# Performance work log

Hardware: AMD Instinct MI355X
Metric: run time of the kernel (lower is better)

The kernel has to match this reference:

```python
import jax, jax.numpy as jnp
import numpy as np

EPS = 1e-5
K = 2  # superpatch hop


def _bn(x, gamma, beta, mean, var):
    # inference-mode BatchNorm2d over channel dim (NCHW)
    inv = gamma / jnp.sqrt(var + EPS)
    return x * inv[None, :, None, None] + (beta - mean * inv)[None, :, None, None]


def _conv1x1(x, w, b):
    # x: [B,C,H,W], w: [O,C], b: [O]
    return jnp.einsum('bchw,oc->bohw', x, w) + b[None, :, None, None]


def setup_inputs() -> dict:
    key = jax.random.key(0)
    ks = jax.random.split(key, 24)
    B, C, H, W = 32, 192, 56, 56
    r = lambda k, shape, s=0.05: jax.random.normal(k, shape, dtype=jnp.float32) * s
    pv = lambda k, shape: jax.random.uniform(k, shape, dtype=jnp.float32, minval=0.5, maxval=1.5)
    inp = {
        'x': jax.random.normal(ks[0], (B, C, H, W), dtype=jnp.float32),
        # RepCPE: depthwise 7x7 conv, groups=C -> weight [C,1,7,7]
        'cpe_w': r(ks[1], (C, 1, 7, 7)),
        'cpe_b': r(ks[2], (C,)),
        # fc1: 1x1 conv C->C + BN
        'fc1_w': r(ks[3], (C, C)), 'fc1_b': r(ks[4], (C,)),
        'bn1_g': pv(ks[5], (C,)), 'bn1_b': r(ks[6], (C,)),
        'bn1_m': r(ks[7], (C,), 0.1), 'bn1_v': pv(ks[8], (C,)),
        # graph_conv.nn: 1x1 conv 2C->C + BN + GELU
        'gc_w': r(ks[9], (C, 2 * C)), 'gc_b': r(ks[10], (C,)),
        'bng_g': pv(ks[11], (C,)), 'bng_b': r(ks[12], (C,)),
        'bng_m': r(ks[13], (C,), 0.1), 'bng_v': pv(ks[14], (C,)),
        # fc2: 1x1 conv C->C + BN
        'fc2_w': r(ks[15], (C, C)), 'fc2_b': r(ks[16], (C,)),
        'bn2_g': pv(ks[17], (C,)), 'bn2_b': r(ks[18], (C,)),
        'bn2_m': r(ks[19], (C,), 0.1), 'bn2_v': pv(ks[20], (C,)),
    }
    return inp


def reference(x, cpe_w, cpe_b, fc1_w, fc1_b, bn1_g, bn1_b, bn1_m, bn1_v,
              gc_w, gc_b, bng_g, bng_b, bng_m, bng_v,
              fc2_w, fc2_b, bn2_g, bn2_b, bn2_m, bn2_v):
    C = x.shape[1]
    # --- RepCPE: depthwise 7x7 conv + bias, residual add ---
    pe = jax.lax.conv_general_dilated(
        x, cpe_w, window_strides=(1, 1), padding='SAME',
        feature_group_count=C,
        dimension_numbers=('NCHW', 'OIHW', 'NCHW'))
    x = pe + cpe_b[None, :, None, None] + x
    # --- fc1: 1x1 conv + BN ---
    x = _bn(_conv1x1(x, fc1_w, fc1_b), bn1_g, bn1_b, bn1_m, bn1_v)
    # --- MRConv4d: max-relative over 4 shifted neighbor views ---
    # torch.cat([x[..., -K:, :], x[..., :-K, :]], dim=2) == roll(+K) along H, etc.
    d = jnp.maximum(jnp.roll(x, K, axis=2) - x, jnp.roll(x, -K, axis=2) - x)
    d = jnp.maximum(d, jnp.roll(x, K, axis=3) - x)
    x_j = jnp.maximum(jnp.maximum(d, jnp.roll(x, -K, axis=3) - x), 0.0)  # x_j init = x - x = 0
    xc = jnp.concatenate([x, x_j], axis=1)  # [B,2C,H,W]
    x = jax.nn.gelu(_bn(_conv1x1(xc, gc_w, gc_b), bng_g, bng_b, bng_m, bng_v),
                    approximate=False)
    # --- fc2: 1x1 conv + BN ---
    x = _bn(_conv1x1(x, fc2_w, fc2_b), bn2_g, bn2_b, bn2_m, bn2_v)
    return x
```

## Files before the change

kernel.cpp:

```cpp
#include <hip/hip_runtime.h>
#include <hip/hip_bf16.h>


#define CC   192
#define HW   3136
#define NB   32

using short8 = __attribute__((ext_vector_type(8))) short;
using f32x4  = __attribute__((ext_vector_type(4))) float;

__device__ __forceinline__ float bf2f(short s) {
  union { unsigned u; float f; } x; x.u = ((unsigned)(unsigned short)s) << 16; return x.f;
}
__device__ __forceinline__ short f2bf(float f) {
  __hip_bfloat16 h = __float2bfloat16(f);
  return *reinterpret_cast<short*>(&h);
}
__device__ __forceinline__ float geluf(float v) {
  float u = 0.7978845608028654f * (v + 0.044715f * v * v * v);
  float e = __expf(2.0f * u);
  return 0.5f * v * (2.0f - 2.0f / (e + 1.0f));
}
__device__ __forceinline__ void gl2lds(const char* g, char* l) {
  __builtin_amdgcn_global_load_lds(
      (const __attribute__((address_space(1))) void*)g,
      (__attribute__((address_space(3))) void*)l, 16, 0, 0);
}

__global__ void __launch_bounds__(256) fold_kernel(
    const float* __restrict__ fc1_w, const float* __restrict__ fc1_b,
    const float* __restrict__ bn1_g, const float* __restrict__ bn1_b,
    const float* __restrict__ bn1_m, const float* __restrict__ bn1_v,
    const float* __restrict__ gc_w,  const float* __restrict__ gc_b,
    const float* __restrict__ bng_g, const float* __restrict__ bng_b,
    const float* __restrict__ bng_m, const float* __restrict__ bng_v,
    const float* __restrict__ fc2_w, const float* __restrict__ fc2_b,
    const float* __restrict__ bn2_g, const float* __restrict__ bn2_b,
    const float* __restrict__ bn2_m, const float* __restrict__ bn2_v,
    __hip_bfloat16* __restrict__ W1f, __hip_bfloat16* __restrict__ Wgf, __hip_bfloat16* __restrict__ W2f,
    float* __restrict__ b1f, float* __restrict__ bgf, float* __restrict__ b2f) {
  int gt = blockIdx.x * 256 + threadIdx.x;
  if (gt < 3 * CC) {
    int which = gt / CC, o = gt - which * CC;
    const float *G, *Bt, *M, *V, *Bi; float* dst;
    if (which == 0)      { G = bn1_g; Bt = bn1_b; M = bn1_m; V = bn1_v; Bi = fc1_b; dst = b1f; }
    else if (which == 1) { G = bng_g; Bt = bng_b; M = bng_m; V = bng_v; Bi = gc_b;  dst = bgf; }
    else                 { G = bn2_g; Bt = bn2_b; M = bn2_m; V = bn2_v; Bi = fc2_b; dst = b2f; }
    float inv = G[o] * rsqrtf(V[o] + 1e-5f);
    dst[o] = Bi[o] * inv + Bt[o] - M[o] * inv;
  }
  int i = gt;
  if (i < CC * CC) {
    int o = i / CC;
    float inv = bn1_g[o] * rsqrtf(bn1_v[o] + 1e-5f);
    W1f[i] = __float2bfloat16(fc1_w[i] * inv);
  } else if (i < CC * CC + CC * 2 * CC) {
    int j = i - CC * CC; int o = j / (2 * CC);
    float inv = bng_g[o] * rsqrtf(bng_v[o] + 1e-5f);
    Wgf[j] = __float2bfloat16(gc_w[j] * inv);
  } else if (i < CC * CC * 4) {
    int j = i - CC * CC * 3; int o = j / CC;
    float inv = bn2_g[o] * rsqrtf(bn2_v[o] + 1e-5f);
    W2f[j] = __float2bfloat16(fc2_w[j] * inv);
  }
}

#define CSTR 956
__global__ void __launch_bounds__(256, 4) dwconv_kernel(
    const float* __restrict__ x, const float* __restrict__ cw,
    const float* __restrict__ cb, __hip_bfloat16* __restrict__ y0pm) {
  __shared__ short in_t[16 * CSTR];
  const int t = threadIdx.x;
  int bb = blockIdx.x;
  const int rs = bb % 7;  bb /= 7;
  const int cg = bb % 12; bb /= 12;
  const int b  = bb;
  const int h0 = rs * 8;

  for (int i = t; i < 16 * CSTR / 8; i += 256) ((int4*)in_t)[i] = int4{0, 0, 0, 0};
  __syncthreads();

  for (int it = t; it < 16 * 14 * 14; it += 256) {
    int w4 = it % 14, rr = (it / 14) % 14, c = it / 196;
    int gh = h0 - 3 + rr;
    if (gh >= 0 && gh < 56) {
      float4 v = *(const float4*)(x + ((size_t)(b * CC + cg * 16 + c) * 56 + gh) * 56 + w4 * 4);
      short4 s4 = { f2bf(v.x), f2bf(v.y), f2bf(v.z), f2bf(v.w) };
      *(short4*)(in_t + c * CSTR + rr * 68 + 4 + w4 * 4) = s4;
    }
  }
  __syncthreads();

  const int c = t & 15, g = t >> 4;
  const int cgx = g % 7, rh = g / 7;
  if (g < 14) {
    const float* wp = cw + (cg * 16 + c) * 49;
    const float bias = cb[cg * 16 + c];
    const short* base = in_t + c * CSTR + rh * 4 * 68 + cgx * 8;
    float acc[4][8] = {};
    float wr[7], wn[7];
#pragma unroll
    for (int i = 0; i < 7; ++i) wr[i] = wp[i];
#pragma unroll
    for (int kh = 0; kh < 7; ++kh) {
      if (kh < 6) {
#pragma unroll
        for (int i = 0; i < 7; ++i) wn[i] = wp[(kh + 1) * 7 + i];
      }
      if (kh == 3) wr[3] += 1.0f;
#pragma unroll
      for (int r = 0; r < 4; ++r) {
        const short* rp = base + (r + kh) * 68;
        int2 q0 = *(const int2*)(rp);
        int2 q1 = *(const int2*)(rp + 4);
        int2 q2 = *(const int2*)(rp + 8);
        int2 q3 = *(const int2*)(rp + 12);
        int dw[8] = { q0.x, q0.y, q1.x, q1.y, q2.x, q2.y, q3.x, q3.y };
        float v[16];
#pragma unroll
        for (int q = 0; q < 8; ++q) {
          union { int i; float f; } lo, hi;
          lo.i = dw[q] << 16; hi.i = dw[q] & 0xffff0000;
          v[q * 2] = lo.f; v[q * 2 + 1] = hi.f;
        }
#pragma unroll
        for (int kw = 0; kw < 7; ++kw) {
          float wv = wr[kw];
#pragma unroll
          for (int ww = 0; ww < 8; ++ww)
            acc[r][ww] = fmaf(wv, v[ww + kw + 1], acc[r][ww]);
        }
      }
#pragma unroll
      for (int i = 0; i < 7; ++i) wr[i] = wn[i];
    }
    short* dst = (short*)y0pm + ((size_t)b * HW + (size_t)(h0 + rh * 4) * 56 + cgx * 8) * CC
                 + cg * 16 + c;
#pragma unroll
    for (int r = 0; r < 4; ++r)
#pragma unroll
      for (int ww = 0; ww < 8; ++ww)
        dst[(size_t)(r * 56 + ww) * CC] = f2bf(acc[r][ww] + bias);
  }
}

__device__ __forceinline__ void xj_load(short8 (&nb)[5], const short* y1c, int hwl) {
  int h = hwl / 56, w = hwl - h * 56;
  int hp = (h >= 54) ? h - 54 : h + 2;
  int hm = (h < 2) ? h + 54 : h - 2;
  int wp = (w >= 54) ? w - 54 : w + 2;
  int wm = (w < 2) ? w + 54 : w - 2;
  nb[0] = *(const short8*)(y1c + (size_t)hwl * CC);
  nb[1] = *(const short8*)(y1c + (size_t)(hp * 56 + w) * CC);
  nb[2] = *(const short8*)(y1c + (size_t)(hm * 56 + w) * CC);
  nb[3] = *(const short8*)(y1c + (size_t)(h * 56 + wp) * CC);
  nb[4] = *(const short8*)(y1c + (size_t)(h * 56 + wm) * CC);
}
__device__ __forceinline__ void xj_write(char* dst, const short8 (&nb)[5], int dstoff) {
  short8 res;
#pragma unroll
  for (int q = 0; q < 8; ++q) {
    float m = fmaxf(fmaxf(bf2f(nb[1][q]), bf2f(nb[2][q])),
                    fmaxf(bf2f(nb[3][q]), bf2f(nb[4][q])));
    res[q] = f2bf(fmaxf(m - bf2f(nb[0][q]), 0.0f));
  }
  *(short8*)(dst + dstoff) = res;
}

template<int MODE>
__global__ void __launch_bounds__(256, 2) gemm_kernel(
    const __hip_bfloat16* __restrict__ actA,
    const __hip_bfloat16* __restrict__ Wf, const float* __restrict__ bfv,
    void* __restrict__ outp) {
  __shared__ char smem[2][24576];
  const int t = threadIdx.x;
  const int lane = t & 63, w = t >> 6;
  const int lrow = lane & 15, lhi = lane >> 4;
  constexpr int NT = NB * 49;

  int goff[6];
#pragma unroll
  for (int j = 0; j < 6; ++j) {
    int idx = j * 4096 + t * 16;
    int p = idx / 384, qd = idx - p * 384;
    goff[j] = p * 384 + (qd ^ ((p & 7) << 4));
  }

  float bw0[3];
  float bw2[3][4];
  if (MODE != 2) {
#pragma unroll
    for (int wi = 0; wi < 3; ++wi) bw0[wi] = bfv[w * 48 + wi * 16 + lrow];
  } else {
#pragma unroll
    for (int wi = 0; wi < 3; ++wi)
#pragma unroll
      for (int r = 0; r < 4; ++r) bw2[wi][r] = bfv[w * 48 + wi * 16 + lhi * 4 + r];
  }

  short8 wreg[6][3];
#pragma unroll
  for (int kk = 0; kk < 6; ++kk)
#pragma unroll
    for (int wi = 0; wi < 3; ++wi) {
      int o = w * 48 + wi * 16 + lrow;
      wreg[kk][wi] = *(const short8*)((const short*)Wf + (size_t)o * 192 + kk * 32 + lhi * 8);
    }

  const int step = gridDim.x;
  int tile = blockIdx.x;
  {
    const char* src = (const char*)actA + (size_t)tile * 24576;
#pragma unroll
    for (int j = 0; j < 6; ++j)
      gl2lds(src + goff[j], smem[0] + j * 4096 + w * 1024);
  }
  __syncthreads();
  int cur = 0;

  while (tile < NT) {
    const int tnext = tile + step;
    f32x4 acc[4][3] = {};
    if (tnext < NT) {
      const char* nsrc = (const char*)actA + (size_t)tnext * 24576;
#pragma unroll
      for (int j = 0; j < 6; ++j)
        gl2lds(nsrc + goff[j], smem[cur ^ 1] + j * 4096 + w * 1024);
    }
#pragma unroll
    for (int kk = 0; kk < 6; ++kk) {
      short8 af[4];
#pragma unroll
      for (int ai = 0; ai < 4; ++ai) {
        int p = ai * 16 + lrow;
        af[ai] = *(const short8*)(smem[cur] + p * 384 + ((kk * 64 + lhi * 16) ^ ((p & 7) << 4)));
      }
#pragma unroll
      for (int ai = 0; ai < 4; ++ai)
#pragma unroll
        for (int wi = 0; wi < 3; ++wi)
          acc[ai][wi] = (MODE == 2)
              ? __builtin_amdgcn_mfma_f32_16x16x32_bf16(wreg[kk][wi], af[ai], acc[ai][wi], 0, 0, 0)
              : __builtin_amdgcn_mfma_f32_16x16x32_bf16(af[ai], wreg[kk][wi], acc[ai][wi], 0, 0, 0);
    }
    __syncthreads();
    cur ^= 1;

    if (MODE != 2) {
      short* ob = (short*)outp + (size_t)tile * 64 * CC;
#pragma unroll
      for (int wi = 0; wi < 3; ++wi) {
        int o = w * 48 + wi * 16 + lrow;
#pragma unroll
        for (int ai = 0; ai < 4; ++ai)
#pragma unroll
          for (int r = 0; r < 4; ++r) {
            int p = ai * 16 + lhi * 4 + r;
            ob[(size_t)p * CC + o] = f2bf(acc[ai][wi][r] + bw0[wi]);
          }
      }
    } else {
      int bimg = tile / 49, hwbase = (tile - bimg * 49) * 64;
      float* ob = (float*)outp + (size_t)bimg * CC * HW + hwbase;
#pragma unroll
      for (int wi = 0; wi < 3; ++wi)
#pragma unroll
        for (int r = 0; r < 4; ++r) {
          int o = w * 48 + wi * 16 + lhi * 4 + r;
#pragma unroll
          for (int ai = 0; ai < 4; ++ai)
            ob[(size_t)o * HW + ai * 16 + lrow] = acc[ai][wi][r] + bw2[wi][r];
        }
    }
    tile = tnext;
  }
}

__global__ void __launch_bounds__(768, 3) gemm2_kernel(
    const __hip_bfloat16* __restrict__ y1g, const __hip_bfloat16* __restrict__ Wf,
    const float* __restrict__ bfv, __hip_bfloat16* __restrict__ outp) {
  __shared__ char smem[2][24576];
  const int t = threadIdx.x;
  const int lane = t & 63, w = t >> 6;
  const int lrow = lane & 15, lhi = lane >> 4;
  constexpr int NT = NB * 49;

  int sp[2], sq[2], goff[2];
#pragma unroll
  for (int j = 0; j < 2; ++j) {
    int idx = j * 12288 + t * 16;
    sp[j] = idx / 384;
    sq[j] = idx - sp[j] * 384;
    goff[j] = sp[j] * 384 + (sq[j] ^ ((sp[j] & 7) << 4));
  }

  const float bw = bfv[w * 16 + lrow];

  short8 wreg[2][6];
#pragma unroll
  for (int c = 0; c < 2; ++c)
#pragma unroll
    for (int kk = 0; kk < 6; ++kk) {
      int o = w * 16 + lrow;
      wreg[c][kk] = *(const short8*)((const short*)Wf +
          (size_t)o * 384 + c * 192 + kk * 32 + lhi * 8);
    }

  const int step = gridDim.x;
  int tile = blockIdx.x;
  {
    const char* src = (const char*)y1g + (size_t)tile * 24576;
#pragma unroll
    for (int j = 0; j < 2; ++j)
      gl2lds(src + goff[j], smem[0] + j * 12288 + w * 1024);
  }
  __syncthreads();
  int cur = 0;

  while (tile < NT) {
    const int tnext = tile + step;
    const int bimg = tile / 49;
    const int hwbase = (tile - bimg * 49) * 64;
    const short* y1b = (const short*)y1g + (size_t)bimg * HW * CC;
    f32x4 acc[4] = {};

#pragma unroll
    for (int j = 0; j < 2; ++j) {
      short8 nb[5];
      xj_load(nb, y1b + (sq[j] >> 1), hwbase + sp[j]);
      xj_write(smem[cur ^ 1], nb, goff[j]);
    }
#pragma unroll
    for (int kk = 0; kk < 6; ++kk) {
      short8 af[4];
#pragma unroll
      for (int ai = 0; ai < 4; ++ai) {
        int p = ai * 16 + lrow;
        af[ai] = *(const short8*)(smem[cur] + p * 384 + ((kk * 64 + lhi * 16) ^ ((p & 7) << 4)));
      }
#pragma unroll
      for (int ai = 0; ai < 4; ++ai)
        acc[ai] = __builtin_amdgcn_mfma_f32_16x16x32_bf16(af[ai], wreg[0][kk], acc[ai], 0, 0, 0);
    }
    __syncthreads();
    cur ^= 1;

    if (tnext < NT) {
      const char* nsrc = (const char*)y1g + (size_t)tnext * 24576;
#pragma unroll
      for (int j = 0; j < 2; ++j)
        gl2lds(nsrc + goff[j], smem[cur ^ 1] + j * 12288 + w * 1024);
    }
#pragma unroll
    for (int kk = 0; kk < 6; ++kk) {
      short8 af[4];
#pragma unroll
      for (int ai = 0; ai < 4; ++ai) {
        int p = ai * 16 + lrow;
        af[ai] = *(const short8*)(smem[cur] + p * 384 + ((kk * 64 + lhi * 16) ^ ((p & 7) << 4)));
      }
#pragma unroll
      for (int ai = 0; ai < 4; ++ai)
        acc[ai] = __builtin_amdgcn_mfma_f32_16x16x32_bf16(af[ai], wreg[1][kk], acc[ai], 0, 0, 0);
    }
    __syncthreads();
    cur ^= 1;

    short* ob = (short*)outp + (size_t)tile * 64 * CC;
    const int o = w * 16 + lrow;
#pragma unroll
    for (int ai = 0; ai < 4; ++ai)
#pragma unroll
      for (int r = 0; r < 4; ++r) {
        int p = ai * 16 + lhi * 4 + r;
        ob[(size_t)p * CC + o] = f2bf(geluf(acc[ai][r] + bw));
      }
    tile = tnext;
  }
}

extern "C" void kernel_launch(void* const* d_in, const int* in_sizes, int n_in,
                              void* d_out, int out_size, void* d_ws, size_t ws_size,
                              hipStream_t stream) {
  const float* x     = (const float*)d_in[0];
  const float* cpe_w = (const float*)d_in[1];
  const float* cpe_b = (const float*)d_in[2];
  const float* fc1_w = (const float*)d_in[3];
  const float* fc1_b = (const float*)d_in[4];
  const float* bn1_g = (const float*)d_in[5];
  const float* bn1_b = (const float*)d_in[6];
  const float* bn1_m = (const float*)d_in[7];
  const float* bn1_v = (const float*)d_in[8];
  const float* gc_w  = (const float*)d_in[9];
  const float* gc_b  = (const float*)d_in[10];
  const float* bng_g = (const float*)d_in[11];
  const float* bng_b = (const float*)d_in[12];
  const float* bng_m = (const float*)d_in[13];
  const float* bng_v = (const float*)d_in[14];
  const float* fc2_w = (const float*)d_in[15];
  const float* fc2_b = (const float*)d_in[16];
  const float* bn2_g = (const float*)d_in[17];
  const float* bn2_b = (const float*)d_in[18];
  const float* bn2_m = (const float*)d_in[19];
  const float* bn2_v = (const float*)d_in[20];

  if (ws_size < 77594624) return;
  char* ws = (char*)d_ws;
  __hip_bfloat16* W1f = (__hip_bfloat16*)(ws);
  __hip_bfloat16* Wgf = (__hip_bfloat16*)(ws + 73728);
  __hip_bfloat16* W2f = (__hip_bfloat16*)(ws + 221184);
  float* b1f = (float*)(ws + 294912);
  float* bgf = (float*)(ws + 295680);
  float* b2f = (float*)(ws + 296448);
  __hip_bfloat16* y0  = (__hip_bfloat16*)(ws + 524288);
  __hip_bfloat16* y1  = (__hip_bfloat16*)d_out;
  float* out = (float*)d_out;

  fold_kernel<<<576, 256, 0, stream>>>(fc1_w, fc1_b, bn1_g, bn1_b, bn1_m, bn1_v,
      gc_w, gc_b, bng_g, bng_b, bng_m, bng_v, fc2_w, fc2_b, bn2_g, bn2_b, bn2_m, bn2_v,
      W1f, Wgf, W2f, b1f, bgf, b2f);
  dwconv_kernel<<<NB * 12 * 7, 256, 0, stream>>>(x, cpe_w, cpe_b, y0);
  gemm_kernel<0><<<512, 256, 0, stream>>>(y0, W1f, b1f, y1);
  gemm2_kernel<<<512, 768, 0, stream>>>(y1, Wgf, bgf, y0);
  gemm_kernel<2><<<512, 256, 0, stream>>>(y0, W2f, b2f, out);
}
```

Baseline: 146.4 us.

## Pack channel pairs in LDS and use packed FP32 FMA in depthwise conv

The depthwise 7x7 conv kernel now stores two channels interleaved as bf16 pairs per 32-bit LDS word and computes both channels at once with v_pk_fma_f32 through inline asm. Each thread handles a channel pair over 2 rows by 8 columns instead of one channel over 4 rows, and 224 of the 256 threads do work instead of 224 before. The aim is to halve the FMA instruction count, widen LDS reads, and write output as packed 32-bit stores. The cost is more LDS reads per output, since each thread covers fewer rows and the 6 halo rows are reloaded more often relative to the outputs produced.

```diff
diff --git a/kernel.cpp b/kernel.cpp
--- a/kernel.cpp
+++ b/kernel.cpp
@@ -8,6 +8,7 @@
 
 using short8 = __attribute__((ext_vector_type(8))) short;
 using f32x4  = __attribute__((ext_vector_type(4))) float;
+using f32x2  = __attribute__((ext_vector_type(2))) float;
 
 __device__ __forceinline__ float bf2f(short s) {
   union { unsigned u; float f; } x; x.u = ((unsigned)(unsigned short)s) << 16; return x.f;
@@ -15,6 +16,19 @@
 __device__ __forceinline__ short f2bf(float f) {
   __hip_bfloat16 h = __float2bfloat16(f);
   return *reinterpret_cast<short*>(&h);
+}
+__device__ __forceinline__ unsigned pack_bf2(float a, float b) {
+  return ((unsigned)(unsigned short)f2bf(a)) | (((unsigned)(unsigned short)f2bf(b)) << 16);
+}
+__device__ __forceinline__ f32x2 up2(unsigned d) {
+  union { unsigned u; float f; } lo, hi;
+  lo.u = d << 16; hi.u = d & 0xffff0000u;
+  f32x2 r; r.x = lo.f; r.y = hi.f; return r;
+}
+__device__ __forceinline__ f32x2 pk_fma(f32x2 a, f32x2 b, f32x2 c) {
+  f32x2 d;
+  asm("v_pk_fma_f32 %0, %1, %2, %3" : "=v"(d) : "v"(a), "v"(b), "v"(c));
+  return d;
 }
 __device__ __forceinline__ float geluf(float v) {
   float u = 0.7978845608028654f * (v + 0.044715f * v * v * v);
@@ -65,11 +79,10 @@
   }
 }
 
-#define CSTR 956
 __global__ void __launch_bounds__(256, 4) dwconv_kernel(
     const float* __restrict__ x, const float* __restrict__ cw,
     const float* __restrict__ cb, __hip_bfloat16* __restrict__ y0pm) {
-  __shared__ short in_t[16 * CSTR];
+  __shared__ unsigned in_t2[8 * 956];
   const int t = threadIdx.x;
   int bb = blockIdx.x;
   const int rs = bb % 7;  bb /= 7;
@@ -77,70 +90,77 @@
   const int b  = bb;
   const int h0 = rs * 8;
 
-  for (int i = t; i < 16 * CSTR / 8; i += 256) ((int4*)in_t)[i] = int4{0, 0, 0, 0};
+  for (int i = t; i < 1912; i += 256) ((uint4*)in_t2)[i] = uint4{0, 0, 0, 0};
   __syncthreads();
 
-  for (int it = t; it < 16 * 14 * 14; it += 256) {
-    int w4 = it % 14, rr = (it / 14) % 14, c = it / 196;
+  for (int it = t; it < 8 * 14 * 14; it += 256) {
+    int w4 = it % 14, rr = (it / 14) % 14, cp = it / 196;
     int gh = h0 - 3 + rr;
     if (gh >= 0 && gh < 56) {
-      float4 v = *(const float4*)(x + ((size_t)(b * CC + cg * 16 + c) * 56 + gh) * 56 + w4 * 4);
-      short4 s4 = { f2bf(v.x), f2bf(v.y), f2bf(v.z), f2bf(v.w) };
-      *(short4*)(in_t + c * CSTR + rr * 68 + 4 + w4 * 4) = s4;
+      const float* pa = x + ((size_t)(b * CC + cg * 16 + cp * 2) * 56 + gh) * 56 + w4 * 4;
+      float4 va = *(const float4*)pa;
+      float4 vb = *(const float4*)(pa + 3136);
+      uint4 u;
+      u.x = pack_bf2(va.x, vb.x); u.y = pack_bf2(va.y, vb.y);
+      u.z = pack_bf2(va.z, vb.z); u.w = pack_bf2(va.w, vb.w);
+      *(uint4*)(in_t2 + cp * 956 + rr * 68 + 4 + w4 * 4) = u;
     }
   }
   __syncthreads();
 
-  const int c = t & 15, g = t >> 4;
-  const int cgx = g % 7, rh = g / 7;
-  if (g < 14) {
-    const float* wp = cw + (cg * 16 + c) * 49;
-    const float bias = cb[cg * 16 + c];
-    const short* base = in_t + c * CSTR + rh * 4 * 68 + cgx * 8;
-    float acc[4][8] = {};
-    float wr[7], wn[7];
-#pragma unroll
-    for (int i = 0; i < 7; ++i) wr[i] = wp[i];
+  const int cp = t & 7, g = t >> 3;
+  const int cgx = g % 7, rq = g / 7;
+  if (g < 28) {
+    const float* wpA = cw + (cg * 16 + cp * 2) * 49;
+    f32x2 bias2;
+    bias2.x = cb[cg * 16 + cp * 2];
+    bias2.y = cb[cg * 16 + cp * 2 + 1];
+    const unsigned* base = in_t2 + cp * 956 + rq * 2 * 68 + cgx * 8;
+    f32x2 acc2[2][8] = {};
+    f32x2 wr2[7], wn2[7];
+#pragma unroll
+    for (int i = 0; i < 7; ++i) { wr2[i].x = wpA[i]; wr2[i].y = wpA[49 + i]; }
 #pragma unroll
     for (int kh = 0; kh < 7; ++kh) {
       if (kh < 6) {
 #pragma unroll
-        for (int i = 0; i < 7; ++i) wn[i] = wp[(kh + 1) * 7 + i];
-      }
-      if (kh == 3) wr[3] += 1.0f;
-#pragma unroll
-      for (int r = 0; r < 4; ++r) {
-        const short* rp = base + (r + kh) * 68;
-        int2 q0 = *(const int2*)(rp);
-        int2 q1 = *(const int2*)(rp + 4);
-        int2 q2 = *(const int2*)(rp + 8);
-        int2 q3 = *(const int2*)(rp + 12);
-        int dw[8] = { q0.x, q0.y, q1.x, q1.y, q2.x, q2.y, q3.x, q3.y };
-        float v[16];
-#pragma unroll
-        for (int q = 0; q < 8; ++q) {
-          union { int i; float f; } lo, hi;
-          lo.i = dw[q] << 16; hi.i = dw[q] & 0xffff0000;
-          v[q * 2] = lo.f; v[q * 2 + 1] = hi.f;
+        for (int i = 0; i < 7; ++i) {
+          wn2[i].x = wpA[(kh + 1) * 7 + i];
+          wn2[i].y = wpA[49 + (kh + 1) * 7 + i];
         }
+      }
+      if (kh == 3) { wr2[3].x += 1.0f; wr2[3].y += 1.0f; }
+#pragma unroll
+      for (int r = 0; r < 2; ++r) {
+        const unsigned* rp = base + (r + kh) * 68;
+        uint4 d0 = *(const uint4*)(rp);
+        uint4 d1 = *(const uint4*)(rp + 4);
+        uint4 d2 = *(const uint4*)(rp + 8);
+        uint4 d3 = *(const uint4*)(rp + 12);
+        unsigned dw[16] = { d0.x, d0.y, d0.z, d0.w, d1.x, d1.y, d1.z, d1.w,
+                            d2.x, d2.y, d2.z, d2.w, d3.x, d3.y, d3.z, d3.w };
+        f32x2 v2[16];
+#pragma unroll
+        for (int q = 0; q < 16; ++q) v2[q] = up2(dw[q]);
 #pragma unroll
         for (int kw = 0; kw < 7; ++kw) {
-          float wv = wr[kw];
 #pragma unroll
           for (int ww = 0; ww < 8; ++ww)
-            acc[r][ww] = fmaf(wv, v[ww + kw + 1], acc[r][ww]);
+            acc2[r][ww] = pk_fma(wr2[kw], v2[ww + kw + 1], acc2[r][ww]);
         }
       }
 #pragma unroll
-      for (int i = 0; i < 7; ++i) wr[i] = wn[i];
-    }
-    short* dst = (short*)y0pm + ((size_t)b * HW + (size_t)(h0 + rh * 4) * 56 + cgx * 8) * CC
-                 + cg * 16 + c;
-#pragma unroll
-    for (int r = 0; r < 4; ++r)
-#pragma unroll
-      for (int ww = 0; ww < 8; ++ww)
-        dst[(size_t)(r * 56 + ww) * CC] = f2bf(acc[r][ww] + bias);
+      for (int i = 0; i < 7; ++i) wr2[i] = wn2[i];
+    }
+    short* dst0 = (short*)y0pm + ((size_t)b * HW + (size_t)(h0 + rq * 2) * 56 + cgx * 8) * CC
+                  + cg * 16 + cp * 2;
+#pragma unroll
+    for (int r = 0; r < 2; ++r)
+#pragma unroll
+      for (int ww = 0; ww < 8; ++ww) {
+        unsigned pv = pack_bf2(acc2[r][ww].x + bias2.x, acc2[r][ww].y + bias2.y);
+        *(unsigned*)(dst0 + (size_t)(r * 56 + ww) * CC) = pv;
+      }
   }
 }
 
```

Result: faster. 140.9 us (-3.8%).
